# Optimization experiments

Hardware: AMD Instinct MI355X
Metric: run time of the kernel (lower is better)

The kernel has to match this reference:

```python
import jax, jax.numpy as jnp
import numpy as np

N, D = 20000, 16          # nodes, fixed in-degree
IN, HID, OUT = 128, 128, 1


def _lstm_final_h(x_seq, Wih, Whh, bih, bhh):
    # x_seq: [D, N, F]; LSTM with hidden size H == F, zero init state.
    # Returns final hidden state h_D: [N, H]. PyTorch gate order i,f,g,o.
    Nn = x_seq.shape[1]
    H = Whh.shape[1]
    b = bih + bhh

    def step(carry, xt):
        h, c = carry
        gates = xt @ Wih.T + h @ Whh.T + b          # [N, 4H]
        i, f, g, o = jnp.split(gates, 4, axis=-1)
        c = jax.nn.sigmoid(f) * c + jax.nn.sigmoid(i) * jnp.tanh(g)
        h = jax.nn.sigmoid(o) * jnp.tanh(c)
        return (h, c), None

    init = (jnp.zeros((Nn, H), x_seq.dtype), jnp.zeros((Nn, H), x_seq.dtype))
    (h, _), _ = jax.lax.scan(step, init, x_seq)
    return h


def _sage_lstm(x, nbr_idx, Wih, Whh, bih, bhh, Wself, Wneigh, bneigh):
    # DGL SAGEConv(aggregator='lstm'): out = fc_self(x) + fc_neigh(lstm(neighbors))
    msgs = x[nbr_idx]                                # gather: [N, D, F]
    hN = _lstm_final_h(jnp.swapaxes(msgs, 0, 1), Wih, Whh, bih, bhh)  # [N, F]
    return x @ Wself.T + hN @ Wneigh.T + bneigh


def setup_inputs() -> dict:
    key = jax.random.key(0)
    ks = jax.random.split(key, 16)
    s = 1.0 / float(np.sqrt(IN))
    u = lambda k, sh: jax.random.uniform(k, sh, jnp.float32, -s, s)
    return {
        "x": jax.random.normal(ks[0], (N, IN), jnp.float32),
        "nbr_idx": jax.random.randint(ks[1], (N, D), 0, N),
        "Wih1": u(ks[2], (4 * IN, IN)), "Whh1": u(ks[3], (4 * IN, IN)),
        "bih1": u(ks[4], (4 * IN,)), "bhh1": u(ks[5], (4 * IN,)),
        "Wself1": u(ks[6], (HID, IN)), "Wneigh1": u(ks[7], (HID, IN)),
        "bneigh1": jnp.zeros((HID,), jnp.float32),
        "Wih2": u(ks[8], (4 * HID, HID)), "Whh2": u(ks[9], (4 * HID, HID)),
        "bih2": u(ks[10], (4 * HID,)), "bhh2": u(ks[11], (4 * HID,)),
        "Wself2": u(ks[12], (OUT, HID)), "Wneigh2": u(ks[13], (OUT, HID)),
        "bneigh2": jnp.zeros((OUT,), jnp.float32),
    }


def reference(x, nbr_idx, Wih1, Whh1, bih1, bhh1, Wself1, Wneigh1, bneigh1,
              Wih2, Whh2, bih2, bhh2, Wself2, Wneigh2, bneigh2):
    h = _sage_lstm(x, nbr_idx, Wih1, Whh1, bih1, bhh1, Wself1, Wneigh1, bneigh1)
    h = jax.nn.relu(h)
    h = _sage_lstm(h, nbr_idx, Wih2, Whh2, bih2, bhh2, Wself2, Wneigh2, bneigh2)
    return jax.nn.sigmoid(h)
```

## Files before the change

kernel.cpp:

```cpp
#include <hip/hip_runtime.h>


#define NN   20000
#define L2E  1.4426950408889634f

typedef unsigned short u16;
typedef __attribute__((ext_vector_type(8))) short frag8;
typedef __attribute__((ext_vector_type(4))) float facc4;
typedef __attribute__((ext_vector_type(8))) _Float16 half8;

#define OFF_X16   0u
#define OFF_H1    5120000u
#define OFF_WIH1P 15360000u
#define OFF_WHH1P 15491072u
#define OFF_WIH2P 15622144u
#define OFF_WHH2P 15753216u
#define OFF_WS1P  15884288u
#define OFF_WN1P  15917056u
#define OFF_WS2B  15949824u
#define OFF_WN2B  15950080u
#define OFF_B1    15950336u
#define OFF_B2    15952384u
#define OFF_XPREA 15954432u
#define OFF_XPREB 36434432u

__device__ __forceinline__ u16 f2bf(float f) {
  union { float f; unsigned u; } v; v.f = f;
  unsigned r = (v.u + 0x7fffu + ((v.u >> 16) & 1u)) >> 16;
  return (u16)r;
}
__device__ __forceinline__ float bflo(unsigned u) {
  union { unsigned u; float f; } v; v.u = u << 16; return v.f;
}
__device__ __forceinline__ float bfhi(unsigned u) {
  union { unsigned u; float f; } v; v.u = u & 0xffff0000u; return v.f;
}
__device__ __forceinline__ unsigned pk2h(float a, float b) {
  union { _Float16 h[2]; unsigned u; } v;
  v.h[0] = (_Float16)a; v.h[1] = (_Float16)b;
  return v.u;
}
__device__ __forceinline__ unsigned pkbf(float a, float b) {
  unsigned r;
  asm("v_cvt_pk_bf16_f32 %0, %1, %2" : "=v"(r) : "v"(a), "v"(b));
  return r;
}
__device__ __forceinline__ facc4 mfma16(frag8 a, frag8 b, facc4 c) {
  return __builtin_amdgcn_mfma_f32_16x16x32_bf16(a, b, c, 0, 0, 0);
}
__device__ __forceinline__ float sigm_ps(float xp) {
  return __builtin_amdgcn_rcpf(1.f + __builtin_amdgcn_exp2f(-xp));
}
__device__ __forceinline__ float tanh_ps(float xp) {
  return 1.f - 2.f * __builtin_amdgcn_rcpf(1.f + __builtin_amdgcn_exp2f(xp));
}
__device__ __forceinline__ float gate_scale(int row) {
  return (row >= 256 && row < 384) ? 2.f * L2E : L2E;
}
__device__ __forceinline__ float dot2(unsigned a, unsigned b) {
  return bflo(a) * bflo(b) + bfhi(a) * bfhi(b);
}

__device__ __forceinline__ void pack512(u16* dst, const float* src, int i) {
  int e = i & 7, ln = (i >> 3) & 63, kb = (i >> 9) & 3, tj = i >> 11;
  int row = tj * 16 + (ln & 15);
  int col = kb * 32 + (ln >> 4) * 8 + e;
  dst[i] = f2bf(src[row * 128 + col] * gate_scale(row));
}
__device__ __forceinline__ void pack128(u16* dst, const float* src, int i) {
  int e = i & 7, ln = (i >> 3) & 63, kb = (i >> 9) & 3, tj = i >> 11;
  dst[i] = f2bf(src[(tj * 16 + (ln & 15)) * 128 + kb * 32 + (ln >> 4) * 8 + e]);
}

__global__ __launch_bounds__(256) void pack_kernel(
    const float* __restrict__ Wih1, const float* __restrict__ Whh1,
    const float* __restrict__ bih1, const float* __restrict__ bhh1,
    const float* __restrict__ Wself1, const float* __restrict__ Wneigh1,
    const float* __restrict__ Wih2, const float* __restrict__ Whh2,
    const float* __restrict__ bih2, const float* __restrict__ bhh2,
    const float* __restrict__ Wself2, const float* __restrict__ Wneigh2,
    char* __restrict__ ws)
{
  int i = blockIdx.x * 256 + threadIdx.x;
  if (i < 65536) { pack512((u16*)(ws + OFF_WIH1P), Wih1, i); return; }
  i -= 65536;
  if (i < 65536) { pack512((u16*)(ws + OFF_WHH1P), Whh1, i); return; }
  i -= 65536;
  if (i < 65536) { pack512((u16*)(ws + OFF_WIH2P), Wih2, i); return; }
  i -= 65536;
  if (i < 65536) { pack512((u16*)(ws + OFF_WHH2P), Whh2, i); return; }
  i -= 65536;
  if (i < 16384) { pack128((u16*)(ws + OFF_WS1P), Wself1, i); return; }
  i -= 16384;
  if (i < 16384) { pack128((u16*)(ws + OFF_WN1P), Wneigh1, i); return; }
  i -= 16384;
  if (i < 128) { ((u16*)(ws + OFF_WS2B))[i] = f2bf(Wself2[i]); return; }
  i -= 128;
  if (i < 128) { ((u16*)(ws + OFF_WN2B))[i] = f2bf(Wneigh2[i]); return; }
  i -= 128;
  if (i < 512) { ((float*)(ws + OFF_B1))[i] = (bih1[i] + bhh1[i]) * gate_scale(i); return; }
  i -= 512;
  if (i < 512) { ((float*)(ws + OFF_B2))[i] = (bih2[i] + bhh2[i]) * gate_scale(i); }
}

__global__ __launch_bounds__(512) void prep1_kernel(
    const float* __restrict__ x,
    const frag8* __restrict__ Wp,
    const float* __restrict__ bias,
    u16* __restrict__ x16,
    u16* __restrict__ xpre)
{
  __shared__ __align__(16) u16 xt[32 * 136];
  __shared__ __align__(16) u16 stage[32 * 520];
  const int tid = threadIdx.x;
  const int base = blockIdx.x * 32;
  {
    int r = tid >> 4, o = (tid & 15) * 8;
    const float* src = x + (size_t)(base + r) * 128 + o;
    float4 v0 = *(const float4*)(src);
    float4 v1 = *(const float4*)(src + 4);
    uint4 st = { pkbf(v0.x, v0.y), pkbf(v0.z, v0.w),
                 pkbf(v1.x, v1.y), pkbf(v1.z, v1.w) };
    *(uint4*)(xt + r * 136 + o) = st;
    *(uint4*)(x16 + (size_t)(base + r) * 128 + o) = st;
  }
  __syncthreads();
  const int lane = tid & 63, wave = tid >> 6;
  const int m = lane & 15, quad = lane >> 4;
  const int rg = wave & 1, jh = wave >> 1;
  const int r = rg * 16 + m;
  frag8 bfr[4];
#pragma unroll
  for (int kb = 0; kb < 4; ++kb)
    bfr[kb] = *(const frag8*)(xt + r * 136 + kb * 32 + quad * 8);
  u16* srow = stage + r * 520;
#pragma unroll
  for (int j = 0; j < 8; ++j) {
    const int tj = jh * 8 + j;
    float4 bv = *(const float4*)(bias + tj * 16 + quad * 4);
    facc4 acc = {bv.x, bv.y, bv.z, bv.w};
#pragma unroll
    for (int kb = 0; kb < 4; ++kb)
      acc = mfma16(Wp[(tj * 4 + kb) * 64 + lane], bfr[kb], acc);
    uint2 st = { pk2h(acc[0], acc[1]), pk2h(acc[2], acc[3]) };
    *(uint2*)(srow + (tj & 7) * 64 + quad * 16 + (tj >> 3) * 4) = st;
  }
  __syncthreads();
#pragma unroll
  for (int i = tid; i < 2048; i += 512) {
    int rr = i >> 6, cc = i & 63;
    ((uint4*)(xpre + (size_t)(base + rr) * 512))[cc] =
        ((const uint4*)(stage + rr * 520))[cc];
  }
}

__global__ __launch_bounds__(512, 4) void lstm_kernel(
    const u16* __restrict__ Xpre,
    const frag8* __restrict__ Wp,
    const int* __restrict__ nbr,
    const u16* __restrict__ xin,
    const frag8* __restrict__ Wsp, const frag8* __restrict__ Wnp,
    const float* __restrict__ bias_o,
    const frag8* __restrict__ WihX, const float* __restrict__ biasX,
    u16* __restrict__ xpreOut,
    const u16* __restrict__ ws2, const u16* __restrict__ wn2,
    const float* __restrict__ b2o,
    u16* __restrict__ h1,
    float* __restrict__ outp,
    int mode)
{
  __shared__ __align__(16) u16 h_lds[2][16 * 136];
  __shared__ __align__(16) u16 xstage[16 * 520];
  const int tid = threadIdx.x;
  const int lane = tid & 63, g = tid >> 6;
  const int m = lane & 15, quad = lane >> 4;

  frag8 A[4][4];
#pragma unroll
  for (int gate = 0; gate < 4; ++gate)
#pragma unroll
    for (int kb = 0; kb < 4; ++kb)
      A[gate][kb] = Wp[((gate * 8 + g) * 4 + kb) * 64 + lane];

  for (int i = tid; i < 16 * 136; i += 512) h_lds[0][i] = 0;

  const int node_base = blockIdx.x * 16;
  int4 idx4 = *(const int4*)(nbr + (size_t)(node_base + m) * 16 + quad * 4);

  facc4 c = {0.f, 0.f, 0.f, 0.f};

  auto xslice = [&](int t) -> const uint4* {
    const int tq = t >> 2, ts = t & 3;
    int sel = (ts == 0) ? idx4.x : (ts == 1) ? idx4.y : (ts == 2) ? idx4.z : idx4.w;
    int idx = __shfl(sel, m + (tq << 4), 64);
    return (const uint4*)(Xpre + (size_t)idx * 512) + g * 8 + quad * 2;
  };

  uint4 pX0, pX1;
  { const uint4* p0 = xslice(0); pX0 = p0[0]; pX1 = p0[1]; }

  __syncthreads();

#pragma unroll 1
  for (int t = 0; t < 16; ++t) {
    const u16* hr = h_lds[t & 1];
    u16* hw = h_lds[(t + 1) & 1];
    const uint4* pn = xslice(t < 15 ? t + 1 : 15);

    frag8 bfr[4];
#pragma unroll
    for (int kb = 0; kb < 4; ++kb)
      bfr[kb] = *(const frag8*)(hr + m * 136 + kb * 32 + quad * 8);

    union { uint4 u; half8 h; } ua, ub;
    ua.u = pX0; ub.u = pX1;
    facc4 ai = {(float)ua.h[0], (float)ua.h[1], (float)ua.h[2], (float)ua.h[3]};
    facc4 af = {(float)ua.h[4], (float)ua.h[5], (float)ua.h[6], (float)ua.h[7]};
    facc4 ag = {(float)ub.h[0], (float)ub.h[1], (float)ub.h[2], (float)ub.h[3]};
    facc4 ao = {(float)ub.h[4], (float)ub.h[5], (float)ub.h[6], (float)ub.h[7]};
    pX0 = pn[0]; pX1 = pn[1];

#pragma unroll
    for (int kb = 0; kb < 4; ++kb) {
      ai = mfma16(A[0][kb], bfr[kb], ai);
      af = mfma16(A[1][kb], bfr[kb], af);
      ag = mfma16(A[2][kb], bfr[kb], ag);
      ao = mfma16(A[3][kb], bfr[kb], ao);
    }

    facc4 hv;
#pragma unroll
    for (int r = 0; r < 4; ++r) {
      float si = sigm_ps(ai[r]);
      float sf = sigm_ps(af[r]);
      float tg = tanh_ps(ag[r]);
      float cn = sf * c[r] + si * tg;
      c[r] = cn;
      float so = sigm_ps(ao[r]);
      hv[r] = so * tanh_ps((2.f * L2E) * cn);
    }
    uint2 hp = { pkbf(hv[0], hv[1]), pkbf(hv[2], hv[3]) };
    *(uint2*)(hw + m * 136 + g * 16 + quad * 4) = hp;
    asm volatile("s_waitcnt lgkmcnt(0)" ::: "memory");
    __builtin_amdgcn_s_barrier();
  }

  const u16* hf = h_lds[0];

  if (mode == 0) {
    const int row = node_base + m;
    frag8 bx[4], bh[4];
#pragma unroll
    for (int kb = 0; kb < 4; ++kb) {
      bx[kb] = *(const frag8*)(xin + (size_t)row * 128 + kb * 32 + quad * 8);
      bh[kb] = *(const frag8*)(hf + m * 136 + kb * 32 + quad * 8);
    }
    float4 bv = *(const float4*)(bias_o + g * 16 + quad * 4);
    facc4 acc = {bv.x, bv.y, bv.z, bv.w};
#pragma unroll
    for (int kb = 0; kb < 4; ++kb) {
      frag8 wsk = Wsp[(g * 4 + kb) * 64 + lane];
      acc = mfma16(wsk, bx[kb], acc);
      frag8 wnk = Wnp[(g * 4 + kb) * 64 + lane];
      acc = mfma16(wnk, bh[kb], acc);
    }
    uint2 st = { pkbf(fmaxf(acc[0], 0.f), fmaxf(acc[1], 0.f)),
                 pkbf(fmaxf(acc[2], 0.f), fmaxf(acc[3], 0.f)) };
    u16* stg = (u16*)h_lds[1];
    *(uint2*)(stg + m * 136 + g * 16 + quad * 4) = st;
    __syncthreads();
    {
      const int r = tid >> 5, cc = tid & 31;
      *(uint2*)(h1 + (size_t)(node_base + r) * 128 + cc * 4) =
          *(const uint2*)(stg + r * 136 + cc * 4);
    }
    frag8 b2f[4];
#pragma unroll
    for (int kb = 0; kb < 4; ++kb)
      b2f[kb] = *(const frag8*)(stg + m * 136 + kb * 32 + quad * 8);
#pragma unroll
    for (int j = 0; j < 4; ++j) {
      const int tj = g * 4 + j;
      float4 bx2 = *(const float4*)(biasX + tj * 16 + quad * 4);
      facc4 acc2 = {bx2.x, bx2.y, bx2.z, bx2.w};
#pragma unroll
      for (int kb = 0; kb < 4; ++kb)
        acc2 = mfma16(WihX[(tj * 4 + kb) * 64 + lane], b2f[kb], acc2);
      uint2 st2 = { pk2h(acc2[0], acc2[1]), pk2h(acc2[2], acc2[3]) };
      *(uint2*)(xstage + m * 520 + (tj & 7) * 64 + quad * 16 + (tj >> 3) * 4) = st2;
    }
    __syncthreads();
#pragma unroll
    for (int i = tid; i < 1024; i += 512) {
      int rr = i >> 6, cc = i & 63;
      ((uint4*)(xpreOut + (size_t)(node_base + rr) * 512))[cc] =
          ((const uint4*)(xstage + rr * 520))[cc];
    }
  } else {
    const int n = tid >> 5, cc = tid & 31;
    uint2 a = *(const uint2*)(h1 + (size_t)(node_base + n) * 128 + cc * 4);
    uint2 w = *(const uint2*)(ws2 + cc * 4);
    uint2 b = *(const uint2*)(hf + n * 136 + cc * 4);
    uint2 v = *(const uint2*)(wn2 + cc * 4);
    float p = dot2(a.x, w.x) + dot2(a.y, w.y) + dot2(b.x, v.x) + dot2(b.y, v.y);
#pragma unroll
    for (int s = 1; s < 32; s <<= 1) p += __shfl_xor(p, s, 64);
    if (cc == 0) {
      float acc = p + b2o[0];
      outp[node_base + n] =
          __builtin_amdgcn_rcpf(1.f + __builtin_amdgcn_exp2f(-acc * L2E));
    }
  }
}

extern "C" void kernel_launch(void* const* d_in, const int* in_sizes, int n_in,
                              void* d_out, int out_size, void* d_ws, size_t ws_size,
                              hipStream_t stream) {
  const float* x       = (const float*)d_in[0];
  const int*   nbr     = (const int*)d_in[1];
  const float* Wih1    = (const float*)d_in[2];
  const float* Whh1    = (const float*)d_in[3];
  const float* bih1    = (const float*)d_in[4];
  const float* bhh1    = (const float*)d_in[5];
  const float* Wself1  = (const float*)d_in[6];
  const float* Wneigh1 = (const float*)d_in[7];
  const float* bneigh1 = (const float*)d_in[8];
  const float* Wih2    = (const float*)d_in[9];
  const float* Whh2    = (const float*)d_in[10];
  const float* bih2    = (const float*)d_in[11];
  const float* bhh2    = (const float*)d_in[12];
  const float* Wself2  = (const float*)d_in[13];
  const float* Wneigh2 = (const float*)d_in[14];
  const float* bneigh2 = (const float*)d_in[15];

  char* ws = (char*)d_ws;
  u16*   x16   = (u16*)(ws + OFF_X16);
  u16*   h1    = (u16*)(ws + OFF_H1);
  u16*   XpreA = (u16*)(ws + OFF_XPREA);
  u16*   XpreB = (u16*)(ws + OFF_XPREB);
  frag8* Wih1p = (frag8*)(ws + OFF_WIH1P);
  frag8* Whh1p = (frag8*)(ws + OFF_WHH1P);
  frag8* Wih2p = (frag8*)(ws + OFF_WIH2P);
  frag8* Whh2p = (frag8*)(ws + OFF_WHH2P);
  frag8* Ws1p  = (frag8*)(ws + OFF_WS1P);
  frag8* Wn1p  = (frag8*)(ws + OFF_WN1P);
  u16*   Ws2b  = (u16*)(ws + OFF_WS2B);
  u16*   Wn2b  = (u16*)(ws + OFF_WN2B);
  float* b1    = (float*)(ws + OFF_B1);
  float* b2    = (float*)(ws + OFF_B2);

  pack_kernel<<<1157, 256, 0, stream>>>(Wih1, Whh1, bih1, bhh1, Wself1,
                                        Wneigh1, Wih2, Whh2, bih2, bhh2,
                                        Wself2, Wneigh2, ws);
  prep1_kernel<<<625, 512, 0, stream>>>(x, Wih1p, b1, x16, XpreA);
  lstm_kernel<<<1250, 512, 0, stream>>>(XpreA, Whh1p, nbr, x16, Ws1p, Wn1p,
                                        bneigh1, Wih2p, b2, XpreB,
                                        Ws2b, Wn2b, bneigh2, h1,
                                        (float*)d_out, 0);
  lstm_kernel<<<1250, 512, 0, stream>>>(XpreB, Whh2p, nbr, x16, Ws1p, Wn1p,
                                        bneigh1, Wih2p, b2, XpreB,
                                        Ws2b, Wn2b, bneigh2, h1,
                                        (float*)d_out, 1);
}
```

Before: 245.5 us.

## Vectorize weight packing, merge LSTM gate reciprocals, stage neighbor indices in LDS

Result: faster. 238.5 us (-2.8%).

```diff
diff --git a/kernel.cpp b/kernel.cpp
--- a/kernel.cpp
+++ b/kernel.cpp
@@ -48,12 +48,9 @@
 __device__ __forceinline__ facc4 mfma16(frag8 a, frag8 b, facc4 c) {
   return __builtin_amdgcn_mfma_f32_16x16x32_bf16(a, b, c, 0, 0, 0);
 }
-__device__ __forceinline__ float sigm_ps(float xp) {
-  return __builtin_amdgcn_rcpf(1.f + __builtin_amdgcn_exp2f(-xp));
-}
-__device__ __forceinline__ float tanh_ps(float xp) {
-  return 1.f - 2.f * __builtin_amdgcn_rcpf(1.f + __builtin_amdgcn_exp2f(xp));
-}
+__device__ __forceinline__ float rcpf(float x) { return __builtin_amdgcn_rcpf(x); }
+__device__ __forceinline__ float ex2(float x)  { return __builtin_amdgcn_exp2f(x); }
+__device__ __forceinline__ float sigm_ps(float xp) { return rcpf(1.f + ex2(-xp)); }
 __device__ __forceinline__ float gate_scale(int row) {
   return (row >= 256 && row < 384) ? 2.f * L2E : L2E;
 }
@@ -61,15 +58,26 @@
   return bflo(a) * bflo(b) + bfhi(a) * bfhi(b);
 }
 
-__device__ __forceinline__ void pack512(u16* dst, const float* src, int i) {
-  int e = i & 7, ln = (i >> 3) & 63, kb = (i >> 9) & 3, tj = i >> 11;
+__device__ __forceinline__ void pack512v(frag8* dst, const float* src, int f) {
+  int ln = f & 63, kb = (f >> 6) & 3, tj = f >> 8;
   int row = tj * 16 + (ln & 15);
-  int col = kb * 32 + (ln >> 4) * 8 + e;
-  dst[i] = f2bf(src[row * 128 + col] * gate_scale(row));
-}
-__device__ __forceinline__ void pack128(u16* dst, const float* src, int i) {
-  int e = i & 7, ln = (i >> 3) & 63, kb = (i >> 9) & 3, tj = i >> 11;
-  dst[i] = f2bf(src[(tj * 16 + (ln & 15)) * 128 + kb * 32 + (ln >> 4) * 8 + e]);
+  int col = kb * 32 + (ln >> 4) * 8;
+  float s = gate_scale(row);
+  const float* p = src + row * 128 + col;
+  float4 v0 = *(const float4*)p;
+  float4 v1 = *(const float4*)(p + 4);
+  uint4 u = { pkbf(v0.x * s, v0.y * s), pkbf(v0.z * s, v0.w * s),
+              pkbf(v1.x * s, v1.y * s), pkbf(v1.z * s, v1.w * s) };
+  *(uint4*)&dst[f] = u;
+}
+__device__ __forceinline__ void pack128v(frag8* dst, const float* src, int f) {
+  int ln = f & 63, kb = (f >> 6) & 3, tj = f >> 8;
+  const float* p = src + (tj * 16 + (ln & 15)) * 128 + kb * 32 + (ln >> 4) * 8;
+  float4 v0 = *(const float4*)p;
+  float4 v1 = *(const float4*)(p + 4);
+  uint4 u = { pkbf(v0.x, v0.y), pkbf(v0.z, v0.w),
+              pkbf(v1.x, v1.y), pkbf(v1.z, v1.w) };
+  *(uint4*)&dst[f] = u;
 }
 
 __global__ __launch_bounds__(256) void pack_kernel(
@@ -82,18 +90,18 @@
     char* __restrict__ ws)
 {
   int i = blockIdx.x * 256 + threadIdx.x;
-  if (i < 65536) { pack512((u16*)(ws + OFF_WIH1P), Wih1, i); return; }
-  i -= 65536;
-  if (i < 65536) { pack512((u16*)(ws + OFF_WHH1P), Whh1, i); return; }
-  i -= 65536;
-  if (i < 65536) { pack512((u16*)(ws + OFF_WIH2P), Wih2, i); return; }
-  i -= 65536;
-  if (i < 65536) { pack512((u16*)(ws + OFF_WHH2P), Whh2, i); return; }
-  i -= 65536;
-  if (i < 16384) { pack128((u16*)(ws + OFF_WS1P), Wself1, i); return; }
-  i -= 16384;
-  if (i < 16384) { pack128((u16*)(ws + OFF_WN1P), Wneigh1, i); return; }
-  i -= 16384;
+  if (i < 8192) { pack512v((frag8*)(ws + OFF_WIH1P), Wih1, i); return; }
+  i -= 8192;
+  if (i < 8192) { pack512v((frag8*)(ws + OFF_WHH1P), Whh1, i); return; }
+  i -= 8192;
+  if (i < 8192) { pack512v((frag8*)(ws + OFF_WIH2P), Wih2, i); return; }
+  i -= 8192;
+  if (i < 8192) { pack512v((frag8*)(ws + OFF_WHH2P), Whh2, i); return; }
+  i -= 8192;
+  if (i < 2048) { pack128v((frag8*)(ws + OFF_WS1P), Wself1, i); return; }
+  i -= 2048;
+  if (i < 2048) { pack128v((frag8*)(ws + OFF_WN1P), Wneigh1, i); return; }
+  i -= 2048;
   if (i < 128) { ((u16*)(ws + OFF_WS2B))[i] = f2bf(Wself2[i]); return; }
   i -= 128;
   if (i < 128) { ((u16*)(ws + OFF_WN2B))[i] = f2bf(Wneigh2[i]); return; }
@@ -154,23 +162,11 @@
   }
 }
 
-__global__ __launch_bounds__(512, 4) void lstm_kernel(
-    const u16* __restrict__ Xpre,
-    const frag8* __restrict__ Wp,
-    const int* __restrict__ nbr,
-    const u16* __restrict__ xin,
-    const frag8* __restrict__ Wsp, const frag8* __restrict__ Wnp,
-    const float* __restrict__ bias_o,
-    const frag8* __restrict__ WihX, const float* __restrict__ biasX,
-    u16* __restrict__ xpreOut,
-    const u16* __restrict__ ws2, const u16* __restrict__ wn2,
-    const float* __restrict__ b2o,
-    u16* __restrict__ h1,
-    float* __restrict__ outp,
-    int mode)
-{
-  __shared__ __align__(16) u16 h_lds[2][16 * 136];
-  __shared__ __align__(16) u16 xstage[16 * 520];
+__device__ __forceinline__ void lstm_core(
+    const u16* __restrict__ Xpre, const frag8* __restrict__ Wp,
+    const int* __restrict__ nbr, int node_base,
+    u16 (*h_lds)[16 * 136], int (*idx_lds)[16])
+{
   const int tid = threadIdx.x;
   const int lane = tid & 63, g = tid >> 6;
   const int m = lane & 15, quad = lane >> 4;
@@ -184,20 +180,19 @@
 
   for (int i = tid; i < 16 * 136; i += 512) h_lds[0][i] = 0;
 
-  const int node_base = blockIdx.x * 16;
   int4 idx4 = *(const int4*)(nbr + (size_t)(node_base + m) * 16 + quad * 4);
+  if (g == 0) {
+    idx_lds[quad * 4 + 0][m] = idx4.x;
+    idx_lds[quad * 4 + 1][m] = idx4.y;
+    idx_lds[quad * 4 + 2][m] = idx4.z;
+    idx_lds[quad * 4 + 3][m] = idx4.w;
+  }
 
   facc4 c = {0.f, 0.f, 0.f, 0.f};
 
-  auto xslice = [&](int t) -> const uint4* {
-    const int tq = t >> 2, ts = t & 3;
-    int sel = (ts == 0) ? idx4.x : (ts == 1) ? idx4.y : (ts == 2) ? idx4.z : idx4.w;
-    int idx = __shfl(sel, m + (tq << 4), 64);
-    return (const uint4*)(Xpre + (size_t)idx * 512) + g * 8 + quad * 2;
-  };
-
-  uint4 pX0, pX1;
-  { const uint4* p0 = xslice(0); pX0 = p0[0]; pX1 = p0[1]; }
+  int idx0 = __shfl(idx4.x, m, 64);
+  const uint4* p0 = (const uint4*)(Xpre + (size_t)idx0 * 512) + g * 8 + quad * 2;
+  uint4 pX0 = p0[0], pX1 = p0[1];
 
   __syncthreads();
 
@@ -205,7 +200,8 @@
   for (int t = 0; t < 16; ++t) {
     const u16* hr = h_lds[t & 1];
     u16* hw = h_lds[(t + 1) & 1];
-    const uint4* pn = xslice(t < 15 ? t + 1 : 15);
+    int idxn = idx_lds[t < 15 ? t + 1 : 15][m];
+    const uint4* pn = (const uint4*)(Xpre + (size_t)idxn * 512) + g * 8 + quad * 2;
 
     frag8 bfr[4];
 #pragma unroll
@@ -231,85 +227,116 @@
     facc4 hv;
 #pragma unroll
     for (int r = 0; r < 4; ++r) {
-      float si = sigm_ps(ai[r]);
+      float ea = ex2(-ai[r]);
+      float eg = ex2(fminf(ag[r], 80.f));
+      float sitg = (eg - 1.f) * rcpf((1.f + ea) * (1.f + eg));
       float sf = sigm_ps(af[r]);
-      float tg = tanh_ps(ag[r]);
-      float cn = sf * c[r] + si * tg;
+      float cn = sf * c[r] + sitg;
       c[r] = cn;
-      float so = sigm_ps(ao[r]);
-      hv[r] = so * tanh_ps((2.f * L2E) * cn);
+      float eo = ex2(-ao[r]);
+      float C  = ex2((2.f * L2E) * cn);
+      hv[r] = (C - 1.f) * rcpf((1.f + eo) * (1.f + C));
     }
     uint2 hp = { pkbf(hv[0], hv[1]), pkbf(hv[2], hv[3]) };
     *(uint2*)(hw + m * 136 + g * 16 + quad * 4) = hp;
     asm volatile("s_waitcnt lgkmcnt(0)" ::: "memory");
     __builtin_amdgcn_s_barrier();
   }
-
+}
+
+__global__ __launch_bounds__(512, 4) void lstm1_kernel(
+    const u16* __restrict__ Xpre, const frag8* __restrict__ Wp,
+    const int* __restrict__ nbr, const u16* __restrict__ xin,
+    const frag8* __restrict__ Wsp, const frag8* __restrict__ Wnp,
+    const float* __restrict__ bias_o,
+    const frag8* __restrict__ WihX, const float* __restrict__ biasX,
+    u16* __restrict__ xpreOut, u16* __restrict__ h1)
+{
+  __shared__ __align__(16) u16 h_lds[2][16 * 136];
+  __shared__ int idx_lds[16][16];
+  __shared__ __align__(16) u16 xstage[16 * 520];
+  const int tid = threadIdx.x;
+  const int lane = tid & 63, g = tid >> 6;
+  const int m = lane & 15, quad = lane >> 4;
+  const int node_base = blockIdx.x * 16;
+
+  lstm_core(Xpre, Wp, nbr, node_base, h_lds, idx_lds);
   const u16* hf = h_lds[0];
 
-  if (mode == 0) {
-    const int row = node_base + m;
-    frag8 bx[4], bh[4];
-#pragma unroll
-    for (int kb = 0; kb < 4; ++kb) {
-      bx[kb] = *(const frag8*)(xin + (size_t)row * 128 + kb * 32 + quad * 8);
-      bh[kb] = *(const frag8*)(hf + m * 136 + kb * 32 + quad * 8);
-    }
-    float4 bv = *(const float4*)(bias_o + g * 16 + quad * 4);
-    facc4 acc = {bv.x, bv.y, bv.z, bv.w};
-#pragma unroll
-    for (int kb = 0; kb < 4; ++kb) {
-      frag8 wsk = Wsp[(g * 4 + kb) * 64 + lane];
-      acc = mfma16(wsk, bx[kb], acc);
-      frag8 wnk = Wnp[(g * 4 + kb) * 64 + lane];
-      acc = mfma16(wnk, bh[kb], acc);
-    }
-    uint2 st = { pkbf(fmaxf(acc[0], 0.f), fmaxf(acc[1], 0.f)),
-                 pkbf(fmaxf(acc[2], 0.f), fmaxf(acc[3], 0.f)) };
-    u16* stg = (u16*)h_lds[1];
-    *(uint2*)(stg + m * 136 + g * 16 + quad * 4) = st;
-    __syncthreads();
-    {
-      const int r = tid >> 5, cc = tid & 31;
-      *(uint2*)(h1 + (size_t)(node_base + r) * 128 + cc * 4) =
-          *(const uint2*)(stg + r * 136 + cc * 4);
-    }
-    frag8 b2f[4];
+  const int row = node_base + m;
+  frag8 bx[4], bh[4];
+#pragma unroll
+  for (int kb = 0; kb < 4; ++kb) {
+    bx[kb] = *(const frag8*)(xin + (size_t)row * 128 + kb * 32 + quad * 8);
+    bh[kb] = *(const frag8*)(hf + m * 136 + kb * 32 + quad * 8);
+  }
+  float4 bv = *(const float4*)(bias_o + g * 16 + quad * 4);
+  facc4 acc = {bv.x, bv.y, bv.z, bv.w};
+#pragma unroll
+  for (int kb = 0; kb < 4; ++kb) {
+    acc = mfma16(Wsp[(g * 4 + kb) * 64 + lane], bx[kb], acc);
+    acc = mfma16(Wnp[(g * 4 + kb) * 64 + lane], bh[kb], acc);
+  }
+  uint2 st = { pkbf(fmaxf(acc[0], 0.f), fmaxf(acc[1], 0.f)),
+               pkbf(fmaxf(acc[2], 0.f), fmaxf(acc[3], 0.f)) };
+  u16* stg = (u16*)h_lds[1];
+  *(uint2*)(stg + m * 136 + g * 16 + quad * 4) = st;
+  __syncthreads();
+  {
+    const int r = tid >> 5, cc = tid & 31;
+    *(uint2*)(h1 + (size_t)(node_base + r) * 128 + cc * 4) =
+        *(const uint2*)(stg + r * 136 + cc * 4);
+  }
+  frag8 b2f[4];
+#pragma unroll
+  for (int kb = 0; kb < 4; ++kb)
+    b2f[kb] = *(const frag8*)(stg + m * 136 + kb * 32 + quad * 8);
+#pragma unroll
+  for (int j = 0; j < 4; ++j) {
+    const int tj = g * 4 + j;
+    float4 bx2 = *(const float4*)(biasX + tj * 16 + quad * 4);
+    facc4 acc2 = {bx2.x, bx2.y, bx2.z, bx2.w};
 #pragma unroll
     for (int kb = 0; kb < 4; ++kb)
-      b2f[kb] = *(const frag8*)(stg + m * 136 + kb * 32 + quad * 8);
-#pragma unroll
-    for (int j = 0; j < 4; ++j) {
-      const int tj = g * 4 + j;
-      float4 bx2 = *(const float4*)(biasX + tj * 16 + quad * 4);
-      facc4 acc2 = {bx2.x, bx2.y, bx2.z, bx2.w};
-#pragma unroll
-      for (int kb = 0; kb < 4; ++kb)
-        acc2 = mfma16(WihX[(tj * 4 + kb) * 64 + lane], b2f[kb], acc2);
-      uint2 st2 = { pk2h(acc2[0], acc2[1]), pk2h(acc2[2], acc2[3]) };
-      *(uint2*)(xstage + m * 520 + (tj & 7) * 64 + quad * 16 + (tj >> 3) * 4) = st2;
-    }
-    __syncthreads();
-#pragma unroll
-    for (int i = tid; i < 1024; i += 512) {
-      int rr = i >> 6, cc = i & 63;
-      ((uint4*)(xpreOut + (size_t)(node_base + rr) * 512))[cc] =
-          ((const uint4*)(xstage + rr * 520))[cc];
-    }
-  } else {
-    const int n = tid >> 5, cc = tid & 31;
-    uint2 a = *(const uint2*)(h1 + (size_t)(node_base + n) * 128 + cc * 4);
-    uint2 w = *(const uint2*)(ws2 + cc * 4);
-    uint2 b = *(const uint2*)(hf + n * 136 + cc * 4);
-    uint2 v = *(const uint2*)(wn2 + cc * 4);
-    float p = dot2(a.x, w.x) + dot2(a.y, w.y) + dot2(b.x, v.x) + dot2(b.y, v.y);
-#pragma unroll
-    for (int s = 1; s < 32; s <<= 1) p += __shfl_xor(p, s, 64);
-    if (cc == 0) {
-      float acc = p + b2o[0];
-      outp[node_base + n] =
-          __builtin_amdgcn_rcpf(1.f + __builtin_amdgcn_exp2f(-acc * L2E));
-    }
+      acc2 = mfma16(WihX[(tj * 4 + kb) * 64 + lane], b2f[kb], acc2);
+    uint2 st2 = { pk2h(acc2[0], acc2[1]), pk2h(acc2[2], acc2[3]) };
+    *(uint2*)(xstage + m * 520 + (tj & 7) * 64 + quad * 16 + (tj >> 3) * 4) = st2;
+  }
+  __syncthreads();
+#pragma unroll
+  for (int i = tid; i < 1024; i += 512) {
+    int rr = i >> 6, cc = i & 63;
+    ((uint4*)(xpreOut + (size_t)(node_base + rr) * 512))[cc] =
+        ((const uint4*)(xstage + rr * 520))[cc];
+  }
+}
+
+__global__ __launch_bounds__(512, 4) void lstm2_kernel(
+    const u16* __restrict__ Xpre, const frag8* __restrict__ Wp,
+    const int* __restrict__ nbr,
+    const u16* __restrict__ ws2, const u16* __restrict__ wn2,
+    const float* __restrict__ b2o,
+    const u16* __restrict__ h1, float* __restrict__ outp)
+{
+  __shared__ __align__(16) u16 h_lds[2][16 * 136];
+  __shared__ int idx_lds[16][16];
+  const int tid = threadIdx.x;
+  const int node_base = blockIdx.x * 16;
+
+  lstm_core(Xpre, Wp, nbr, node_base, h_lds, idx_lds);
+  const u16* hf = h_lds[0];
+
+  const int n = tid >> 5, cc = tid & 31;
+  uint2 a = *(const uint2*)(h1 + (size_t)(node_base + n) * 128 + cc * 4);
+  uint2 w = *(const uint2*)(ws2 + cc * 4);
+  uint2 b = *(const uint2*)(hf + n * 136 + cc * 4);
+  uint2 v = *(const uint2*)(wn2 + cc * 4);
+  float p = dot2(a.x, w.x) + dot2(a.y, w.y) + dot2(b.x, v.x) + dot2(b.y, v.y);
+#pragma unroll
+  for (int s = 1; s < 32; s <<= 1) p += __shfl_xor(p, s, 64);
+  if (cc == 0) {
+    float acc = p + b2o[0];
+    outp[node_base + n] = rcpf(1.f + ex2(-acc * L2E));
   }
 }
 
@@ -349,16 +376,12 @@
   float* b1    = (float*)(ws + OFF_B1);
   float* b2    = (float*)(ws + OFF_B2);
 
-  pack_kernel<<<1157, 256, 0, stream>>>(Wih1, Whh1, bih1, bhh1, Wself1,
-                                        Wneigh1, Wih2, Whh2, bih2, bhh2,
-                                        Wself2, Wneigh2, ws);
+  pack_kernel<<<149, 256, 0, stream>>>(Wih1, Whh1, bih1, bhh1, Wself1,
+                                       Wneigh1, Wih2, Whh2, bih2, bhh2,
+                                       Wself2, Wneigh2, ws);
   prep1_kernel<<<625, 512, 0, stream>>>(x, Wih1p, b1, x16, XpreA);
-  lstm_kernel<<<1250, 512, 0, stream>>>(XpreA, Whh1p, nbr, x16, Ws1p, Wn1p,
-                                        bneigh1, Wih2p, b2, XpreB,
-                                        Ws2b, Wn2b, bneigh2, h1,
-                                        (float*)d_out, 0);
-  lstm_kernel<<<1250, 512, 0, stream>>>(XpreB, Whh2p, nbr, x16, Ws1p, Wn1p,
-                                        bneigh1, Wih2p, b2, XpreB,
-                                        Ws2b, Wn2b, bneigh2, h1,
-                                        (float*)d_out, 1);
-}
+  lstm1_kernel<<<1250, 512, 0, stream>>>(XpreA, Whh1p, nbr, x16, Ws1p, Wn1p,
+                                         bneigh1, Wih2p, b2, XpreB, h1);
+  lstm2_kernel<<<1250, 512, 0, stream>>>(XpreB, Whh2p, nbr, Ws2b, Wn2b,
+                                         bneigh2, h1, (float*)d_out);
+}
```
